# Kernel optimization log

Measured on AMD Instinct MI355X. Metric: run time of the kernel, lower is better.

## Reference

```python
import jax, jax.numpy as jnp
import numpy as np

B, L, D_MODEL = 16, 512, 768
S, D_LLM = 2048, 4096
H = 8
E = D_MODEL // H  # d_keys = 96


def setup_inputs() -> dict:
    key = jax.random.key(0)
    ks = jax.random.split(key, 10)
    sc_dm = 1.0 / np.sqrt(D_MODEL)
    sc_dl = 1.0 / np.sqrt(D_LLM)
    return {
        "target": jax.random.normal(ks[0], (B, L, D_MODEL), jnp.float32),
        "source": jax.random.normal(ks[1], (S, D_LLM), jnp.float32),
        "Wq": jax.random.normal(ks[2], (D_MODEL, H * E), jnp.float32) * sc_dm,
        "bq": jnp.zeros((H * E,), jnp.float32),
        "Wk": jax.random.normal(ks[3], (D_LLM, H * E), jnp.float32) * sc_dl,
        "bk": jnp.zeros((H * E,), jnp.float32),
        "Wv": jax.random.normal(ks[4], (D_LLM, H * E), jnp.float32) * sc_dl,
        "bv": jnp.zeros((H * E,), jnp.float32),
        "Wo": jax.random.normal(ks[5], (H * E, D_LLM), jnp.float32) * sc_dm,
        "bo": jnp.zeros((D_LLM,), jnp.float32),
    }


def reference(target, source, Wq, bq, Wk, bk, Wv, bv, Wo, bo):
    # Q: (B, L, H, E); K, V: (S, H, E) -- K/V are shared across the batch.
    Q = (target @ Wq + bq).reshape(B, L, H, E)
    K = (source @ Wk + bk).reshape(S, H, E)
    V = (source @ Wv + bv).reshape(S, H, E)
    # scores: (B, H, L, S)
    scores = jnp.einsum('blhe,she->bhls', Q, K) / jnp.sqrt(jnp.asarray(E, Q.dtype))
    attn = jax.nn.softmax(scores, axis=-1)  # dropout is identity in eval mode
    rep = jnp.einsum('bhls,she->blhe', attn, V).reshape(B, L, H * E)
    return rep @ Wo + bo  # (B, L, d_llm)
```

## Files before the change

### kernel.cpp

```cpp
#include <hip/hip_runtime.h>
#include <hip/hip_bf16.h>
#include <stdint.h>

typedef __hip_bfloat16 bf16;
typedef __attribute__((ext_vector_type(8))) short short8;
typedef __attribute__((ext_vector_type(4))) float floatx4;

__device__ __forceinline__ void gll16(const bf16* g, const bf16* lds_base) {
  __builtin_amdgcn_global_load_lds(
      (const __attribute__((address_space(1))) unsigned int*)g,
      (__attribute__((address_space(3))) unsigned int*)lds_base,
      16, 0, 0);
}

__device__ __forceinline__ unsigned pk2(float a, float b) {
  union { __hip_bfloat16 h; unsigned short u; } ca, cb;
  ca.h = __float2bfloat16(a);
  cb.h = __float2bfloat16(b);
  return (unsigned)ca.u | ((unsigned)cb.u << 16);
}

__global__ __launch_bounds__(256) void cvt_trans(const float* __restrict__ t_in,
                                                 const float* __restrict__ s_in,
                                                 const float* __restrict__ Wq,
                                                 const float* __restrict__ Wk,
                                                 const float* __restrict__ Wv,
                                                 const float* __restrict__ Wo,
                                                 bf16* __restrict__ t_out,
                                                 bf16* __restrict__ s_out,
                                                 bf16* __restrict__ WqT,
                                                 bf16* __restrict__ WkvT,
                                                 bf16* __restrict__ WoT) {
  __shared__ float t[32][33];
  int bid = blockIdx.x;
  if (bid < 14336) {
    const float* in;
    bf16* out;
    int i;
    if (bid < 6144) { in = t_in; out = t_out; i = (bid * 256 + threadIdx.x) * 4; }
    else            { in = s_in; out = s_out; i = ((bid - 6144) * 256 + threadIdx.x) * 4; }
    float4 v = *(const float4*)(in + i);
    out[i + 0] = __float2bfloat16(v.x);
    out[i + 1] = __float2bfloat16(v.y);
    out[i + 2] = __float2bfloat16(v.z);
    out[i + 3] = __float2bfloat16(v.w);
    return;
  }
  int id = bid - 14336;
  const float* in; bf16* out; int R, C, cx, ry;
  if (id < 576)        { in = Wq; out = WqT; R = 768;  C = 768;  id -= 0;    cx = id % 24;  ry = id / 24; }
  else if (id < 3648)  { in = Wk; out = WkvT; R = 4096; C = 768; id -= 576;  cx = id % 24;  ry = id / 24; }
  else if (id < 6720)  { in = Wv; out = WkvT + (size_t)768 * 4096; R = 4096; C = 768; id -= 3648; cx = id % 24; ry = id / 24; }
  else                 { in = Wo; out = WoT; R = 768;  C = 4096; id -= 6720; cx = id % 128; ry = id / 128; }
  int tx = threadIdx.x & 31, ty = threadIdx.x >> 5;
  int c0 = cx * 32, r0 = ry * 32;
#pragma unroll
  for (int j = 0; j < 4; ++j)
    t[ty + j * 8][tx] = in[(size_t)(r0 + ty + j * 8) * C + c0 + tx];
  __syncthreads();
#pragma unroll
  for (int j = 0; j < 4; ++j)
    out[(size_t)(c0 + ty + j * 8) * R + r0 + tx] = __float2bfloat16(t[tx][ty + j * 8]);
}

__device__ __forceinline__ void gemm64_core(const bf16* __restrict__ A,
                                            const bf16* __restrict__ BT,
                                            int K, int kbeg, int kend,
                                            int m0, int n0,
                                            bf16* As, bf16* Bs,
                                            floatx4 acc[2][4]) {
  const int tid = threadIdx.x;
  const int w = tid >> 6, lane = tid & 63;
  const int ln = lane & 15, quad = lane >> 4;
  for (int k0 = kbeg; k0 < kend; k0 += 32) {
    __syncthreads();
#pragma unroll
    for (int t = 0; t < 2; ++t) {
      int cidb = (w * 2 + t) * 64;
      int cid = cidb + lane;
      int row = cid >> 2, ko = (cid & 3) * 8;
      gll16(BT + (size_t)(n0 + row) * K + k0 + ko, Bs + cidb * 8);
    }
    {
      int cidb = w * 64;
      int cid = cidb + lane;
      int row = cid >> 2, ko = (cid & 3) * 8;
      gll16(A + (size_t)(m0 + row) * K + k0 + ko, As + cidb * 8);
    }
    __syncthreads();
    const short8* Av = (const short8*)As;
    const short8* Bv = (const short8*)Bs;
    const int wm = w >> 1, wn = w & 1;
    short8 a[2], b[4];
#pragma unroll
    for (int mt = 0; mt < 2; ++mt) a[mt] = Av[(wm * 32 + mt * 16 + ln) * 4 + quad];
#pragma unroll
    for (int nt = 0; nt < 4; ++nt) b[nt] = Bv[(wn * 64 + nt * 16 + ln) * 4 + quad];
#pragma unroll
    for (int mt = 0; mt < 2; ++mt)
#pragma unroll
      for (int nt = 0; nt < 4; ++nt)
        acc[mt][nt] = __builtin_amdgcn_mfma_f32_16x16x32_bf16(a[mt], b[nt], acc[mt][nt], 0, 0, 0);
  }
}

template <int NS>
__global__ __launch_bounds__(256) void qkv_proj(const bf16* __restrict__ tgt,
                                                const bf16* __restrict__ src,
                                                const bf16* __restrict__ WqT,
                                                const bf16* __restrict__ WkvT,
                                                const float* __restrict__ bq,
                                                bf16* __restrict__ Qws,
                                                float* __restrict__ P) {
  __shared__ bf16 As[64 * 32];
  __shared__ bf16 Bs[128 * 32];
  const int tid = threadIdx.x;
  const int w = tid >> 6, lane = tid & 63;
  const int ln = lane & 15, quad = lane >> 4;
  const int wm = w >> 1, wn = w & 1;
  const int id = blockIdx.x;

  floatx4 acc[2][4] = {};

  if (id < 768) {
    const int mb = id & 127, nb = id >> 7;
    const int m0 = mb * 64, n0 = nb * 128;
    gemm64_core(tgt, WqT, 768, 0, 768, m0, n0, As, Bs, acc);
#pragma unroll
    for (int nt = 0; nt < 4; ++nt) {
      int n = n0 + wn * 64 + nt * 16 + ln;
      float bv_ = bq[n];
#pragma unroll
      for (int mt = 0; mt < 2; ++mt)
#pragma unroll
        for (int r = 0; r < 4; ++r) {
          int m = m0 + wm * 32 + mt * 16 + quad * 4 + r;
          Qws[(size_t)m * 768 + n] = __float2bfloat16(acc[mt][nt][r] + bv_);
        }
    }
  } else {
    const int t2 = id - 768;
    const int z = t2 / 384, r2 = t2 % 384;
    const int mb = r2 & 31, nb = r2 >> 5;
    const int m0 = mb * 64, n0 = nb * 128;
    constexpr int KSEG = 4096 / NS;
    const int kbeg = z * KSEG;
    float* Pz = P + (size_t)z * 2048 * 1536;
    gemm64_core(src, WkvT, 4096, kbeg, kbeg + KSEG, m0, n0, As, Bs, acc);
#pragma unroll
    for (int nt = 0; nt < 4; ++nt) {
      int n = n0 + wn * 64 + nt * 16 + ln;
#pragma unroll
      for (int mt = 0; mt < 2; ++mt)
#pragma unroll
        for (int r = 0; r < 4; ++r) {
          int m = m0 + wm * 32 + mt * 16 + quad * 4 + r;
          Pz[(size_t)m * 1536 + n] = acc[mt][nt][r];
        }
    }
  }
}

template <int NS>
__global__ __launch_bounds__(256) void reduce_kv_both(const float* __restrict__ P,
                                                      const float* __restrict__ bk,
                                                      const float* __restrict__ bv,
                                                      bf16* __restrict__ Kws,
                                                      bf16* __restrict__ VTws) {
  __shared__ float t[32][33];
  if (blockIdx.y == 0) {
    int idx = (blockIdx.x * 256 + threadIdx.x) * 4;
    int m = idx / 768, n = idx % 768;
    float4 acc = *(const float4*)(bk + n);
#pragma unroll
    for (int z = 0; z < NS; ++z) {
      float4 a = *(const float4*)(P + (size_t)z * 2048 * 1536 + (size_t)m * 1536 + n);
      acc.x += a.x; acc.y += a.y; acc.z += a.z; acc.w += a.w;
    }
    Kws[(size_t)m * 768 + n + 0] = __float2bfloat16(acc.x);
    Kws[(size_t)m * 768 + n + 1] = __float2bfloat16(acc.y);
    Kws[(size_t)m * 768 + n + 2] = __float2bfloat16(acc.z);
    Kws[(size_t)m * 768 + n + 3] = __float2bfloat16(acc.w);
  } else {
    int tx = threadIdx.x & 31, ty = threadIdx.x >> 5;
    int c0 = (blockIdx.x % 24) * 32;
    int r0 = (blockIdx.x / 24) * 32;
#pragma unroll
    for (int j = 0; j < 4; ++j) {
      size_t off = (size_t)(r0 + ty + j * 8) * 1536 + 768 + c0 + tx;
      float s = 0.f;
#pragma unroll
      for (int z = 0; z < NS; ++z) s += P[off + (size_t)z * 2048 * 1536];
      t[ty + j * 8][tx] = s;
    }
    __syncthreads();
#pragma unroll
    for (int j = 0; j < 4; ++j) {
      int e = c0 + ty + j * 8;
      VTws[(size_t)e * 2048 + r0 + tx] = __float2bfloat16(t[tx][ty + j * 8] + bv[e]);
    }
  }
}

__global__ __launch_bounds__(256) void gemm_wo(const bf16* __restrict__ A,
                                               const bf16* __restrict__ BT,
                                               const float* __restrict__ bias,
                                               float* __restrict__ C) {
  __shared__ bf16 As[128 * 32];
  __shared__ bf16 Bs[128 * 32];
  const int tid = threadIdx.x;
  const int w = tid >> 6, lane = tid & 63;
  const int ln = lane & 15, quad = lane >> 4;
  const int wm = w >> 1, wn = w & 1;
  const int W = blockIdx.x;
  const int cid2 = (W & 7) * 256 + (W >> 3);
  const int bx = cid2 >> 5, by = cid2 & 31;
  const int m0 = bx * 128, n0 = by * 128;
  const int K = 768, ldc = 4096;

  floatx4 acc[4][4] = {};

  for (int k0 = 0; k0 < K; k0 += 32) {
    __syncthreads();
#pragma unroll
    for (int t = 0; t < 2; ++t) {
      int cidb = (w * 2 + t) * 64;
      int cid = cidb + lane;
      int row = cid >> 2, ko = (cid & 3) * 8;
      gll16(A + (size_t)(m0 + row) * K + k0 + ko, As + cidb * 8);
      gll16(BT + (size_t)(n0 + row) * K + k0 + ko, Bs + cidb * 8);
    }
    __syncthreads();
    const short8* Av = (const short8*)As;
    const short8* Bv = (const short8*)Bs;
    short8 a[4], b[4];
#pragma unroll
    for (int mt = 0; mt < 4; ++mt) a[mt] = Av[(wm * 64 + mt * 16 + ln) * 4 + quad];
#pragma unroll
    for (int nt = 0; nt < 4; ++nt) b[nt] = Bv[(wn * 64 + nt * 16 + ln) * 4 + quad];
#pragma unroll
    for (int mt = 0; mt < 4; ++mt)
#pragma unroll
      for (int nt = 0; nt < 4; ++nt)
        acc[mt][nt] = __builtin_amdgcn_mfma_f32_16x16x32_bf16(a[mt], b[nt], acc[mt][nt], 0, 0, 0);
  }

#pragma unroll
  for (int nt = 0; nt < 4; ++nt) {
    int n = n0 + wn * 64 + nt * 16 + ln;
    float bv_ = bias[n];
#pragma unroll
    for (int mt = 0; mt < 4; ++mt)
#pragma unroll
      for (int r = 0; r < 4; ++r) {
        int m = m0 + wm * 64 + mt * 16 + quad * 4 + r;
        C[(size_t)m * ldc + n] = acc[mt][nt][r] + bv_;
      }
  }
}

__global__ __launch_bounds__(256, 4) void attn_kernel(const bf16* __restrict__ Q,
                                                      const bf16* __restrict__ Kt,
                                                      const bf16* __restrict__ VT,
                                                      bf16* __restrict__ rep) {
  __shared__ __align__(16) bf16 Ks[64 * 13 * 8];
  __shared__ __align__(16) bf16 Vs[96 * 9 * 8];
  __shared__ __align__(16) bf16 Ps[64 * 72];
  __shared__ float Rs[2][64];

  const int tid = threadIdx.x, w = tid >> 6, lane = tid & 63;
  const int ln = lane & 15, quad = lane >> 4;
  const int wq = w >> 1, ws = w & 1;
  const int h = blockIdx.x;
  const int yy = blockIdx.y;
  const int b = yy >> 3, qt = yy & 7;

  const bf16* Qg = Q + (size_t)(b * 512 + qt * 64) * 768 + h * 96;
  short8 qf[2][3];
#pragma unroll
  for (int mt = 0; mt < 2; ++mt)
#pragma unroll
    for (int es = 0; es < 3; ++es)
      qf[mt][es] = *(const short8*)(Qg + (size_t)(wq * 32 + mt * 16 + ln) * 768 + (es * 4 + quad) * 8);

  const bf16* Kgh = Kt + h * 96;
  const bf16* Vgh = VT + (size_t)h * 96 * 2048;

  int krow[3], koff[3], vrow[3], voff[3];
#pragma unroll
  for (int t = 0; t < 3; ++t) {
    int cid = t * 256 + tid;
    krow[t] = cid / 12; koff[t] = cid % 12;
    vrow[t] = cid >> 3; voff[t] = cid & 7;
  }

  short8 kreg[3], vreg[3];
#pragma unroll
  for (int t = 0; t < 3; ++t) {
    kreg[t] = *(const short8*)(Kgh + (size_t)krow[t] * 768 + koff[t] * 8);
    vreg[t] = *(const short8*)(Vgh + (size_t)vrow[t] * 2048 + voff[t] * 8);
  }

  floatx4 po[2][3] = {};
  float psum[2] = {};
  const float cexp = 1.4426950408889634f / 9.797958971132712f;

  for (int it = 0; it < 32; ++it) {
    const int s0 = it * 64;
    __syncthreads();

#pragma unroll
    for (int t = 0; t < 3; ++t) {
      *(short8*)(&Ks[(krow[t] * 13 + koff[t]) * 8]) = kreg[t];
      *(short8*)(&Vs[(vrow[t] * 9 + voff[t]) * 8]) = vreg[t];
    }
    if (it < 31) {
#pragma unroll
      for (int t = 0; t < 3; ++t) {
        kreg[t] = *(const short8*)(Kgh + (size_t)(s0 + 64 + krow[t]) * 768 + koff[t] * 8);
        vreg[t] = *(const short8*)(Vgh + (size_t)vrow[t] * 2048 + s0 + 64 + voff[t] * 8);
      }
    }
    __syncthreads();

    floatx4 sacc[2][2] = {};
    const short8* Kv = (const short8*)Ks;
#pragma unroll
    for (int es = 0; es < 3; ++es) {
      short8 kf[2];
#pragma unroll
      for (int ct = 0; ct < 2; ++ct) kf[ct] = Kv[(ws * 32 + ct * 16 + ln) * 13 + es * 4 + quad];
#pragma unroll
      for (int mt = 0; mt < 2; ++mt)
#pragma unroll
        for (int ct = 0; ct < 2; ++ct)
          sacc[mt][ct] = __builtin_amdgcn_mfma_f32_16x16x32_bf16(kf[ct], qf[mt][es], sacc[mt][ct], 0, 0, 0);
    }

#pragma unroll
    for (int mt = 0; mt < 2; ++mt) {
      float rs = 0.f;
#pragma unroll
      for (int ct = 0; ct < 2; ++ct) {
        float p0 = exp2f(sacc[mt][ct][0] * cexp);
        float p1 = exp2f(sacc[mt][ct][1] * cexp);
        float p2 = exp2f(sacc[mt][ct][2] * cexp);
        float p3 = exp2f(sacc[mt][ct][3] * cexp);
        rs += (p0 + p1) + (p2 + p3);
        uint2 uu;
        uu.x = pk2(p0, p1);
        uu.y = pk2(p2, p3);
        *(uint2*)(Ps + (wq * 32 + mt * 16 + ln) * 72 + ws * 32 + ct * 16 + quad * 4) = uu;
      }
      psum[mt] += rs;
    }
    __syncthreads();

    const short8* Pv = (const short8*)Ps;
    const short8* Vv = (const short8*)Vs;
#pragma unroll
    for (int ks = 0; ks < 2; ++ks) {
      short8 pa[2];
#pragma unroll
      for (int mt = 0; mt < 2; ++mt) pa[mt] = Pv[(wq * 32 + mt * 16 + ln) * 9 + ks * 4 + quad];
#pragma unroll
      for (int nt = 0; nt < 3; ++nt) {
        short8 vb = Vv[(ws * 48 + nt * 16 + ln) * 9 + ks * 4 + quad];
#pragma unroll
        for (int mt = 0; mt < 2; ++mt)
          po[mt][nt] = __builtin_amdgcn_mfma_f32_16x16x32_bf16(pa[mt], vb, po[mt][nt], 0, 0, 0);
      }
    }
  }

  float t0 = psum[0], t1 = psum[1];
  t0 += __shfl_xor(t0, 16, 64); t0 += __shfl_xor(t0, 32, 64);
  t1 += __shfl_xor(t1, 16, 64); t1 += __shfl_xor(t1, 32, 64);
  if (lane < 16) {
    Rs[ws][wq * 32 + lane] = t0;
    Rs[ws][wq * 32 + 16 + lane] = t1;
  }
  __syncthreads();

  float linv[2][4];
#pragma unroll
  for (int mt = 0; mt < 2; ++mt)
#pragma unroll
    for (int r = 0; r < 4; ++r) {
      int q = wq * 32 + mt * 16 + quad * 4 + r;
      float v = Rs[0][q] + Rs[1][q];
      linv[mt][r] = 1.f / fmaxf(v, 1e-37f);
    }

  bf16* og = rep + (size_t)(b * 512 + qt * 64) * 768 + h * 96;
#pragma unroll
  for (int mt = 0; mt < 2; ++mt)
#pragma unroll
    for (int nt = 0; nt < 3; ++nt)
#pragma unroll
      for (int r = 0; r < 4; ++r) {
        int row = wq * 32 + mt * 16 + quad * 4 + r;
        int e = ws * 48 + nt * 16 + ln;
        og[(size_t)row * 768 + e] = __float2bfloat16(po[mt][nt][r] * linv[mt][r]);
      }
}

extern "C" void kernel_launch(void* const* d_in, const int* in_sizes, int n_in,
                              void* d_out, int out_size, void* d_ws, size_t ws_size,
                              hipStream_t stream) {
  const float* target = (const float*)d_in[0];
  const float* source = (const float*)d_in[1];
  const float* Wq = (const float*)d_in[2];
  const float* bq = (const float*)d_in[3];
  const float* Wk = (const float*)d_in[4];
  const float* bk = (const float*)d_in[5];
  const float* Wv = (const float*)d_in[6];
  const float* bv = (const float*)d_in[7];
  const float* Wo = (const float*)d_in[8];
  const float* bo = (const float*)d_in[9];
  float* out = (float*)d_out;

  bf16* ws = (bf16*)d_ws;
  bf16* tgt_bf = ws;
  bf16* src_bf = tgt_bf + 6291456;
  bf16* WqT = src_bf + 8388608;
  bf16* WkvT = WqT + 589824;
  bf16* WoT = WkvT + 6291456;
  bf16* Qws = WoT + 3145728;
  bf16* Kws = Qws + 6291456;
  bf16* VTws = Kws + 1572864;
  float* Pkv = (float*)(ws + 34144256);
  const size_t SEG = 2048ull * 1536 * 4;
  const size_t NEED2 = 68288512ull + 2 * SEG;
  bf16* repws = src_bf;

  cvt_trans<<<24128, 256, 0, stream>>>(target, source, Wq, Wk, Wv, Wo,
                                       tgt_bf, src_bf, WqT, WkvT, WoT);

  if (ws_size >= NEED2) {
    qkv_proj<2><<<768 + 768, 256, 0, stream>>>(tgt_bf, src_bf, WqT, WkvT, bq, Qws, Pkv);
    reduce_kv_both<2><<<dim3(1536, 2), 256, 0, stream>>>(Pkv, bk, bv, Kws, VTws);
  } else {
    qkv_proj<1><<<768 + 384, 256, 0, stream>>>(tgt_bf, src_bf, WqT, WkvT, bq, Qws, Pkv);
    reduce_kv_both<1><<<dim3(1536, 2), 256, 0, stream>>>(Pkv, bk, bv, Kws, VTws);
  }

  attn_kernel<<<dim3(8, 128), 256, 0, stream>>>(Qws, Kws, VTws, repws);

  gemm_wo<<<2048, 256, 0, stream>>>(repws, WoT, bo, out);
}
```

Measured before the change: 473.0 us.

## Keep softmax probabilities in registers via permuted K rows, split S across waves

The change stores K rows in a permuted order in LDS so that the score MFMA output layout already matches the A-operand layout of the PV MFMA. P can then be packed straight into registers, which removes the Ps shared buffer and one __syncthreads per iteration. The two waves in each pair now split the S dimension instead of the E dimension, so partial outputs are reduced through LDS at the end. The softmax scale is folded into Q in the projection epilogue, which removes a multiply per exponent. Accumulator registers per wave double (po goes from 2x3 to 2x6), which may affect occupancy.

```diff
diff --git a/kernel.cpp b/kernel.cpp
--- a/kernel.cpp
+++ b/kernel.cpp
@@ -19,6 +19,8 @@
   cb.h = __float2bfloat16(b);
   return (unsigned)ca.u | ((unsigned)cb.u << 16);
 }
+
+#define CEXP 0.14725532312236443f
 
 __global__ __launch_bounds__(256) void cvt_trans(const float* __restrict__ t_in,
                                                  const float* __restrict__ s_in,
@@ -135,7 +137,7 @@
 #pragma unroll
         for (int r = 0; r < 4; ++r) {
           int m = m0 + wm * 32 + mt * 16 + quad * 4 + r;
-          Qws[(size_t)m * 768 + n] = __float2bfloat16(acc[mt][nt][r] + bv_);
+          Qws[(size_t)m * 768 + n] = __float2bfloat16((acc[mt][nt][r] + bv_) * CEXP);
         }
     }
   } else {
@@ -265,7 +267,6 @@
                                                       bf16* __restrict__ rep) {
   __shared__ __align__(16) bf16 Ks[64 * 13 * 8];
   __shared__ __align__(16) bf16 Vs[96 * 9 * 8];
-  __shared__ __align__(16) bf16 Ps[64 * 72];
   __shared__ float Rs[2][64];
 
   const int tid = threadIdx.x, w = tid >> 6, lane = tid & 63;
@@ -286,11 +287,14 @@
   const bf16* Kgh = Kt + h * 96;
   const bf16* Vgh = VT + (size_t)h * 96 * 2048;
 
-  int krow[3], koff[3], vrow[3], voff[3];
+  int krow[3], kprow[3], koff[3], vrow[3], voff[3];
 #pragma unroll
   for (int t = 0; t < 3; ++t) {
     int cid = t * 256 + tid;
-    krow[t] = cid / 12; koff[t] = cid % 12;
+    int kr = cid / 12;
+    krow[t] = kr;
+    kprow[t] = (kr & 32) | (((kr >> 2) & 1) << 4) | (((kr >> 3) & 3) << 2) | (kr & 3);
+    koff[t] = cid % 12;
     vrow[t] = cid >> 3; voff[t] = cid & 7;
   }
 
@@ -301,9 +305,8 @@
     vreg[t] = *(const short8*)(Vgh + (size_t)vrow[t] * 2048 + voff[t] * 8);
   }
 
-  floatx4 po[2][3] = {};
+  floatx4 po[2][6] = {};
   float psum[2] = {};
-  const float cexp = 1.4426950408889634f / 9.797958971132712f;
 
   for (int it = 0; it < 32; ++it) {
     const int s0 = it * 64;
@@ -311,7 +314,7 @@
 
 #pragma unroll
     for (int t = 0; t < 3; ++t) {
-      *(short8*)(&Ks[(krow[t] * 13 + koff[t]) * 8]) = kreg[t];
+      *(short8*)(&Ks[(kprow[t] * 13 + koff[t]) * 8]) = kreg[t];
       *(short8*)(&Vs[(vrow[t] * 9 + voff[t]) * 8]) = vreg[t];
     }
     if (it < 31) {
@@ -337,72 +340,78 @@
           sacc[mt][ct] = __builtin_amdgcn_mfma_f32_16x16x32_bf16(kf[ct], qf[mt][es], sacc[mt][ct], 0, 0, 0);
     }
 
+    short8 pa[2];
 #pragma unroll
     for (int mt = 0; mt < 2; ++mt) {
-      float rs = 0.f;
-#pragma unroll
-      for (int ct = 0; ct < 2; ++ct) {
-        float p0 = exp2f(sacc[mt][ct][0] * cexp);
-        float p1 = exp2f(sacc[mt][ct][1] * cexp);
-        float p2 = exp2f(sacc[mt][ct][2] * cexp);
-        float p3 = exp2f(sacc[mt][ct][3] * cexp);
-        rs += (p0 + p1) + (p2 + p3);
-        uint2 uu;
-        uu.x = pk2(p0, p1);
-        uu.y = pk2(p2, p3);
-        *(uint2*)(Ps + (wq * 32 + mt * 16 + ln) * 72 + ws * 32 + ct * 16 + quad * 4) = uu;
-      }
-      psum[mt] += rs;
-    }
-    __syncthreads();
-
-    const short8* Pv = (const short8*)Ps;
+      float p0 = exp2f(sacc[mt][0][0]);
+      float p1 = exp2f(sacc[mt][0][1]);
+      float p2 = exp2f(sacc[mt][0][2]);
+      float p3 = exp2f(sacc[mt][0][3]);
+      float p4 = exp2f(sacc[mt][1][0]);
+      float p5 = exp2f(sacc[mt][1][1]);
+      float p6 = exp2f(sacc[mt][1][2]);
+      float p7 = exp2f(sacc[mt][1][3]);
+      psum[mt] += ((p0 + p1) + (p2 + p3)) + ((p4 + p5) + (p6 + p7));
+      union { uint4 u; short8 s; } uu;
+      uu.u.x = pk2(p0, p1);
+      uu.u.y = pk2(p2, p3);
+      uu.u.z = pk2(p4, p5);
+      uu.u.w = pk2(p6, p7);
+      pa[mt] = uu.s;
+    }
+
     const short8* Vv = (const short8*)Vs;
 #pragma unroll
-    for (int ks = 0; ks < 2; ++ks) {
-      short8 pa[2];
-#pragma unroll
-      for (int mt = 0; mt < 2; ++mt) pa[mt] = Pv[(wq * 32 + mt * 16 + ln) * 9 + ks * 4 + quad];
-#pragma unroll
-      for (int nt = 0; nt < 3; ++nt) {
-        short8 vb = Vv[(ws * 48 + nt * 16 + ln) * 9 + ks * 4 + quad];
-#pragma unroll
-        for (int mt = 0; mt < 2; ++mt)
-          po[mt][nt] = __builtin_amdgcn_mfma_f32_16x16x32_bf16(pa[mt], vb, po[mt][nt], 0, 0, 0);
-      }
+    for (int nt = 0; nt < 6; ++nt) {
+      short8 vb = Vv[(nt * 16 + ln) * 9 + ws * 4 + quad];
+#pragma unroll
+      for (int mt = 0; mt < 2; ++mt)
+        po[mt][nt] = __builtin_amdgcn_mfma_f32_16x16x32_bf16(pa[mt], vb, po[mt][nt], 0, 0, 0);
     }
   }
 
   float t0 = psum[0], t1 = psum[1];
   t0 += __shfl_xor(t0, 16, 64); t0 += __shfl_xor(t0, 32, 64);
   t1 += __shfl_xor(t1, 16, 64); t1 += __shfl_xor(t1, 32, 64);
+
+  __syncthreads();
+
   if (lane < 16) {
     Rs[ws][wq * 32 + lane] = t0;
     Rs[ws][wq * 32 + 16 + lane] = t1;
   }
+  float* cb = (wq == 0) ? (float*)Ks : (float*)Vs;
+  if (ws == 0) {
+#pragma unroll
+    for (int mt = 0; mt < 2; ++mt)
+#pragma unroll
+      for (int nt = 0; nt < 6; ++nt)
+#pragma unroll
+        for (int r = 0; r < 4; ++r)
+          cb[(mt * 16 + quad * 4 + r) * 96 + nt * 16 + ln] = po[mt][nt][r];
+  }
   __syncthreads();
 
-  float linv[2][4];
-#pragma unroll
-  for (int mt = 0; mt < 2; ++mt)
-#pragma unroll
-    for (int r = 0; r < 4; ++r) {
-      int q = wq * 32 + mt * 16 + quad * 4 + r;
-      float v = Rs[0][q] + Rs[1][q];
-      linv[mt][r] = 1.f / fmaxf(v, 1e-37f);
-    }
-
-  bf16* og = rep + (size_t)(b * 512 + qt * 64) * 768 + h * 96;
-#pragma unroll
-  for (int mt = 0; mt < 2; ++mt)
-#pragma unroll
-    for (int nt = 0; nt < 3; ++nt)
+  if (ws == 1) {
+    bf16* og = rep + (size_t)(b * 512 + qt * 64) * 768 + h * 96;
+#pragma unroll
+    for (int mt = 0; mt < 2; ++mt) {
+      float linv[4];
 #pragma unroll
       for (int r = 0; r < 4; ++r) {
-        int row = wq * 32 + mt * 16 + quad * 4 + r;
-        int e = ws * 48 + nt * 16 + ln;
-        og[(size_t)row * 768 + e] = __float2bfloat16(po[mt][nt][r] * linv[mt][r]);
+        int q = wq * 32 + mt * 16 + quad * 4 + r;
+        linv[r] = 1.f / fmaxf(Rs[0][q] + Rs[1][q], 1e-37f);
       }
+#pragma unroll
+      for (int nt = 0; nt < 6; ++nt)
+#pragma unroll
+        for (int r = 0; r < 4; ++r) {
+          int row = wq * 32 + mt * 16 + quad * 4 + r;
+          float v = po[mt][nt][r] + cb[(mt * 16 + quad * 4 + r) * 96 + nt * 16 + ln];
+          og[(size_t)row * 768 + nt * 16 + ln] = __float2bfloat16(v * linv[r]);
+        }
+    }
+  }
 }
 
 extern "C" void kernel_launch(void* const* d_in, const int* in_sizes, int n_in,
```

Result: slower. 546.3 us (+15.5%).
